# Kernel optimization log

Measured on AMD Instinct MI355X. Metric: run time of the kernel, lower is better.

## Reference

```python
import jax, jax.numpy as jnp
from jax import lax
import numpy as np

# Dcls2_1d config (matches init_kwargs)
K_H, K_W = 3, 3          # base kernel size
DIL = 4                  # max dilation along dim 0 (learnable spacings)
LIM = DIL // 2           # each tap may move +/- LIM rows
KH_EFF = K_H + 2 * LIM   # constructed kernel height (7)
PAD_H = 1 + LIM          # user padding 1 adjusted by dilation//2 (as in _adjust_padding)
PAD_W = 1


def build_kernel(weight, P1):
    """Construct dense conv kernel by bilinear scatter of weights at
    continuous learnable row offsets P1. weight,P1: (O, I, K_H, K_W).
    Returns (O, I, KH_EFF, K_W)."""
    kh = jnp.arange(K_H, dtype=weight.dtype)[None, None, :, None]
    pos = kh + LIM + jnp.clip(P1, -LIM, LIM)      # continuous row position in [0, KH_EFF-1]
    p0 = jnp.floor(pos)
    frac = pos - p0                                # interpolation residual (grad flows to P)
    p0i = p0.astype(jnp.int32)
    oh0 = jax.nn.one_hot(p0i, KH_EFF, dtype=weight.dtype)        # (O,I,Kh,Kw,KH_EFF)
    oh1 = jax.nn.one_hot(p0i + 1, KH_EFF, dtype=weight.dtype)    # OOB rows -> all-zero row
    return (jnp.einsum('oihw,oihwk->oikw', weight * (1.0 - frac), oh0)
            + jnp.einsum('oihw,oihwk->oikw', weight * frac, oh1))


def setup_inputs() -> dict:
    key = jax.random.key(0)
    k1, k2, k3, k4 = jax.random.split(key, 4)
    x = jax.random.normal(k1, (16, 128, 64, 64), jnp.float32)
    weight = jax.random.normal(k2, (256, 128, 3, 3), jnp.float32) * 0.03
    bias = jax.random.normal(k3, (256,), jnp.float32) * 0.01
    # learnable positions span the allowed +/- LIM range to exercise interpolation
    P = jax.random.uniform(k4, (1, 256, 128, 3, 3), jnp.float32, -2.0, 2.0)
    return {"x": x, "weight": weight, "bias": bias, "P": P}


def reference(x, weight, bias, P):
    K = build_kernel(weight, P[0])
    out = lax.conv_general_dilated(
        x, K,
        window_strides=(1, 1),
        padding=((PAD_H, PAD_H), (PAD_W, PAD_W)),
        dimension_numbers=('NCHW', 'OIHW', 'NCHW'),
        feature_group_count=1)
    return out + bias[None, :, None, None]
```

## Files before the change

kernel.cpp:

```cpp
#include <hip/hip_runtime.h>
#include <hip/hip_bf16.h>

#define NIMG 16
#define CIN 128
#define COUT 256
#define HH 64
#define WW 64
#define KHE 7
#define KW_ 3
#define HP (HH + 6)
#define WP (WW + 2)
#define KDIM (CIN * KHE * KW_)
#define NKT 42

typedef __attribute__((ext_vector_type(8))) short short8;
typedef __attribute__((ext_vector_type(4))) float f32x4;

#define AS1(p) ((const __attribute__((address_space(1))) void*)(p))
#define AS3(p) ((__attribute__((address_space(3))) void*)(p))

__global__ void __launch_bounds__(256) pad_convert(const float* __restrict__ x,
                                                   ushort* __restrict__ xp) {
  const int bid = blockIdx.x;
  const int n = bid / HP, hp = bid % HP;
  const int h = hp - 3;
  ushort* dst = xp + (size_t)(n * HP + hp) * (WP * CIN);
  const int tid = threadIdx.x;

  if (h < 0 || h >= HH) {
    uint4* p = (uint4*)dst;
    uint4 z; z.x = z.y = z.z = z.w = 0u;
    for (int idx = tid; idx < (WP * CIN * 2) / 16; idx += 256) p[idx] = z;
    return;
  }

  __shared__ ushort t[CIN][WW + 1];
  for (int it = 0; it < (CIN * WW) / 256; ++it) {
    int flat = it * 256 + tid;
    int i = flat >> 6, w = flat & 63;
    float v = x[(((size_t)n * CIN + i) * HH + h) * WW + w];
    __hip_bfloat16 b = __float2bfloat16(v);
    t[i][w] = *(ushort*)&b;
  }
  __syncthreads();
  for (int it = 0; it < (WP * CIN) / 256; ++it) {
    int flat = it * 256 + tid;
    int wp = flat >> 7, i = flat & 127;
    int w = wp - 1;
    ushort v = (w < 0 || w >= WW) ? (ushort)0 : t[i][w];
    dst[flat] = v;
  }
}

__global__ void __launch_bounds__(256) build_kb(const float* __restrict__ weight,
                                                const float* __restrict__ P,
                                                ushort* __restrict__ kb) {
  int idx = blockIdx.x * 256 + threadIdx.x;
  if (idx >= COUT * KW_ * CIN) return;
  int i = idx & 127;
  int kw = (idx >> 7) % 3;
  int o = idx / (KW_ * CIN);
  int base = (o * CIN + i) * 9 + kw;

  float a[KHE] = {0.f, 0.f, 0.f, 0.f, 0.f, 0.f, 0.f};
#pragma unroll
  for (int kh = 0; kh < 3; ++kh) {
    float wv = weight[base + kh * 3];
    float p = P[base + kh * 3];
    p = fminf(2.f, fmaxf(-2.f, p));
    float pos = (float)(kh + 2) + p;
    float fl = floorf(pos);
    float fr = pos - fl;
    int r0 = (int)fl;
    float c0 = wv * (1.f - fr);
    float c1 = wv * fr;
#pragma unroll
    for (int r = 0; r < KHE; ++r) {
      a[r] += ((r0 == r) ? c0 : 0.f) + ((r0 + 1 == r) ? c1 : 0.f);
    }
  }
#pragma unroll
  for (int r = 0; r < KHE; ++r) {
    __hip_bfloat16 b = __float2bfloat16(a[r]);
    kb[((size_t)(o * KHE + r) * KW_ + kw) * CIN + i] = *(ushort*)&b;
  }
}

__global__ void __launch_bounds__(512, 2) dcls_gemm(const ushort* __restrict__ xp,
                                                    const ushort* __restrict__ kb,
                                                    const float* __restrict__ bias,
                                                    float* __restrict__ out) {
  __shared__ __align__(16) ushort As[2][256 * 64];
  __shared__ __align__(16) ushort Bs[2][256 * 64];

  const int tid = threadIdx.x;
  const int lane = tid & 63;
  const int wv = tid >> 6;
  const int wr = wv >> 2;
  const int wc = wv & 3;
  const int g = lane >> 4;
  const int lm = lane & 15;
  const int m0 = blockIdx.x << 8;

  const int srow = tid >> 3;
  const int swz = ((tid & 7) ^ (srow & 7)) * 8;

  const ushort* pA[4];
  const ushort* pB[4];
#pragma unroll
  for (int j = 0; j < 4; ++j) {
    int r = j * 64 + srow;
    int m = m0 + r;
    int ni = m >> 12, hh = (m >> 6) & 63, ww = m & 63;
    pA[j] = xp + (size_t)((ni * HP + hh) * WP + ww) * CIN + swz;
    pB[j] = kb + (size_t)r * KDIM + swz;
  }

#define STAGE(c, kt) do { \
    int kh_ = (kt) / 6; int rem_ = (kt) - kh_ * 6; \
    int kw2_ = rem_ >> 1; int ic_ = rem_ & 1; \
    int offA_ = (kh_ * WP + kw2_) * CIN + ic_ * 64; \
    int offB_ = (kh_ * KW_ + kw2_) * CIN + ic_ * 64; \
    _Pragma("unroll") \
    for (int j_ = 0; j_ < 4; ++j_) \
      __builtin_amdgcn_global_load_lds(AS1(pA[j_] + offA_), AS3(&As[c][(j_ * 64 + wv * 8) * 64]), 16, 0, 0); \
    _Pragma("unroll") \
    for (int j_ = 0; j_ < 4; ++j_) \
      __builtin_amdgcn_global_load_lds(AS1(pB[j_] + offB_), AS3(&Bs[c][(j_ * 64 + wv * 8) * 64]), 16, 0, 0); \
  } while (0)

  f32x4 acc[8][4] = {};
  const int swzR = (lm & 7) << 4;

  STAGE(0, 0);
  STAGE(1, 1);

  for (int kt = 0; kt < NKT; ++kt) {
    const int c = kt & 1;
    if (kt < NKT - 1) { asm volatile("s_waitcnt vmcnt(8)" ::: "memory"); }
    else              { asm volatile("s_waitcnt vmcnt(0)" ::: "memory"); }
    __builtin_amdgcn_s_barrier();
    __builtin_amdgcn_sched_barrier(0);

    const char* Ab = (const char*)&As[c][0];
    const char* Bb = (const char*)&Bs[c][0];

    short8 bf[4][2];
#pragma unroll
    for (int n = 0; n < 4; ++n)
#pragma unroll
      for (int kk = 0; kk < 2; ++kk) {
        int rowB = wc * 64 + n * 16 + lm;
        bf[n][kk] = *(const short8*)(Bb + rowB * 128 + ((kk * 64 + g * 16) ^ swzR));
      }

#pragma unroll
    for (int half = 0; half < 2; ++half) {
      short8 af[4][2];
#pragma unroll
      for (int m4 = 0; m4 < 4; ++m4)
#pragma unroll
        for (int kk = 0; kk < 2; ++kk) {
          int rowA = wr * 128 + half * 64 + m4 * 16 + lm;
          af[m4][kk] = *(const short8*)(Ab + rowA * 128 + ((kk * 64 + g * 16) ^ swzR));
        }
#pragma unroll
      for (int kk = 0; kk < 2; ++kk)
#pragma unroll
        for (int m4 = 0; m4 < 4; ++m4)
#pragma unroll
          for (int n = 0; n < 4; ++n)
            acc[half * 4 + m4][n] = __builtin_amdgcn_mfma_f32_16x16x32_bf16(
                af[m4][kk], bf[n][kk], acc[half * 4 + m4][n], 0, 0, 0);
    }

    __builtin_amdgcn_s_barrier();
    __builtin_amdgcn_sched_barrier(0);
    if (kt + 2 < NKT) STAGE(c, kt + 2);
  }
#undef STAGE

#pragma unroll
  for (int fn = 0; fn < 4; ++fn) {
    int o = wc * 64 + fn * 16 + lm;
    float bv = bias[o];
#pragma unroll
    for (int fm = 0; fm < 8; ++fm) {
      int m = m0 + wr * 128 + fm * 16 + g * 4;
      int ni = m >> 12, hh = (m >> 6) & 63, ww = m & 63;
      f32x4 v = acc[fm][fn];
      v[0] += bv; v[1] += bv; v[2] += bv; v[3] += bv;
      *(f32x4*)(out + (size_t)((ni * COUT + o) * HH + hh) * WW + ww) = v;
    }
  }
}

extern "C" void kernel_launch(void* const* d_in, const int* in_sizes, int n_in,
                              void* d_out, int out_size, void* d_ws, size_t ws_size,
                              hipStream_t stream) {
  const float* x = (const float*)d_in[0];
  const float* weight = (const float*)d_in[1];
  const float* bias = (const float*)d_in[2];
  const float* P = (const float*)d_in[3];
  float* out = (float*)d_out;

  const size_t xp_elems = (size_t)NIMG * HP * WP * CIN;
  ushort* xp = (ushort*)d_ws;
  ushort* kb = (ushort*)((char*)d_ws + xp_elems * 2);

  hipLaunchKernelGGL(pad_convert, dim3(NIMG * HP), dim3(256), 0, stream, x, xp);
  hipLaunchKernelGGL(build_kb, dim3((COUT * KW_ * CIN + 255) / 256), dim3(256), 0, stream,
                     weight, P, kb);
  hipLaunchKernelGGL(dcls_gemm, dim3(65536 / 256), dim3(512), 0, stream, xp, kb, bias, out);
}
```

Before: 102.4 us.

## Split GEMM k-tile into four barrier-fenced phases with MFMA priority boost

Breaks each k-tile of the main loop into four phases (two M halves by two K sub-slices). Each phase loads a smaller set of A/B fragments from LDS, waits on LDS, then issues MFMAs at raised wave priority (s_setprio), with block-wide barriers around every phase. The next tile's global-to-LDS stage is issued after all four phases, followed by the vmcnt wait and a barrier. The aim is to shrink fragment register footprint and to interleave LDS reads and MFMA bursts across waves and co-resident blocks. The cost is many more barriers per tile, which may serialize the waves.

New measurement: 114.3 us. 1.12x slower.

```diff
diff --git a/kernel.cpp b/kernel.cpp
--- a/kernel.cpp
+++ b/kernel.cpp
@@ -132,52 +132,66 @@
   f32x4 acc[8][4] = {};
   const int swzR = (lm & 7) << 4;
 
+  short8 bf[4];
+  short8 af[4];
+
+#define PHASE(Ab, Bb, mg, kk, READB) do { \
+    if (READB) { \
+      _Pragma("unroll") \
+      for (int n_ = 0; n_ < 4; ++n_) { \
+        int rowB_ = wc * 64 + n_ * 16 + lm; \
+        bf[n_] = *(const short8*)((Bb) + rowB_ * 128 + (((kk) * 64 + g * 16) ^ swzR)); \
+      } \
+    } \
+    _Pragma("unroll") \
+    for (int m4_ = 0; m4_ < 4; ++m4_) { \
+      int rowA_ = wr * 128 + (mg) * 64 + m4_ * 16 + lm; \
+      af[m4_] = *(const short8*)((Ab) + rowA_ * 128 + (((kk) * 64 + g * 16) ^ swzR)); \
+    } \
+    __builtin_amdgcn_sched_barrier(0); \
+    __builtin_amdgcn_s_barrier(); \
+    asm volatile("s_waitcnt lgkmcnt(0)" ::: "memory"); \
+    __builtin_amdgcn_sched_barrier(0); \
+    __builtin_amdgcn_s_setprio(1); \
+    _Pragma("unroll") \
+    for (int m4_ = 0; m4_ < 4; ++m4_) \
+      _Pragma("unroll") \
+      for (int n_ = 0; n_ < 4; ++n_) \
+        acc[(mg) * 4 + m4_][n_] = __builtin_amdgcn_mfma_f32_16x16x32_bf16( \
+            af[m4_], bf[n_], acc[(mg) * 4 + m4_][n_], 0, 0, 0); \
+    __builtin_amdgcn_s_setprio(0); \
+    __builtin_amdgcn_s_barrier(); \
+  } while (0)
+
   STAGE(0, 0);
   STAGE(1, 1);
+  asm volatile("s_waitcnt vmcnt(8)" ::: "memory");
+  __builtin_amdgcn_sched_barrier(0);
+  __builtin_amdgcn_s_barrier();
 
   for (int kt = 0; kt < NKT; ++kt) {
     const int c = kt & 1;
-    if (kt < NKT - 1) { asm volatile("s_waitcnt vmcnt(8)" ::: "memory"); }
-    else              { asm volatile("s_waitcnt vmcnt(0)" ::: "memory"); }
-    __builtin_amdgcn_s_barrier();
-    __builtin_amdgcn_sched_barrier(0);
-
     const char* Ab = (const char*)&As[c][0];
     const char* Bb = (const char*)&Bs[c][0];
 
-    short8 bf[4][2];
-#pragma unroll
-    for (int n = 0; n < 4; ++n)
-#pragma unroll
-      for (int kk = 0; kk < 2; ++kk) {
-        int rowB = wc * 64 + n * 16 + lm;
-        bf[n][kk] = *(const short8*)(Bb + rowB * 128 + ((kk * 64 + g * 16) ^ swzR));
+    PHASE(Ab, Bb, 0, 0, 1);
+    PHASE(Ab, Bb, 1, 0, 0);
+    PHASE(Ab, Bb, 0, 1, 1);
+    PHASE(Ab, Bb, 1, 1, 0);
+
+    if (kt < NKT - 1) {
+      __builtin_amdgcn_sched_barrier(0);
+      if (kt + 2 < NKT) {
+        STAGE(c, kt + 2);
+        asm volatile("s_waitcnt vmcnt(8)" ::: "memory");
+      } else {
+        asm volatile("s_waitcnt vmcnt(0)" ::: "memory");
       }
-
-#pragma unroll
-    for (int half = 0; half < 2; ++half) {
-      short8 af[4][2];
-#pragma unroll
-      for (int m4 = 0; m4 < 4; ++m4)
-#pragma unroll
-        for (int kk = 0; kk < 2; ++kk) {
-          int rowA = wr * 128 + half * 64 + m4 * 16 + lm;
-          af[m4][kk] = *(const short8*)(Ab + rowA * 128 + ((kk * 64 + g * 16) ^ swzR));
-        }
-#pragma unroll
-      for (int kk = 0; kk < 2; ++kk)
-#pragma unroll
-        for (int m4 = 0; m4 < 4; ++m4)
-#pragma unroll
-          for (int n = 0; n < 4; ++n)
-            acc[half * 4 + m4][n] = __builtin_amdgcn_mfma_f32_16x16x32_bf16(
-                af[m4][kk], bf[n][kk], acc[half * 4 + m4][n], 0, 0, 0);
+      __builtin_amdgcn_sched_barrier(0);
+      __builtin_amdgcn_s_barrier();
     }
-
-    __builtin_amdgcn_s_barrier();
-    __builtin_amdgcn_sched_barrier(0);
-    if (kt + 2 < NKT) STAGE(c, kt + 2);
-  }
+  }
+#undef PHASE
 #undef STAGE
 
 #pragma unroll
```
